# Optimization experiments

Measured on AMD Instinct MI355X. Metric: run time of the kernel, lower is better.

Reference implementation:

```python
import jax, jax.numpy as jnp
import numpy as np

B, C, H, W = 64, 128, 32, 32
GROUPS = 32
EPS = 1e-6
SCALE = 0.044194173824159216  # 1/sqrt(512), as hardcoded in the torch module


def setup_inputs() -> dict:
    key = jax.random.key(0)
    ks = jax.random.split(key, 12)
    s = 1.0 / np.sqrt(C)
    return {
        "x": jax.random.normal(ks[0], (B, C, H, W), dtype=jnp.float32),
        "gn_w": jax.random.normal(ks[1], (C,), dtype=jnp.float32) * 0.02 + 1.0,
        "gn_b": jax.random.normal(ks[2], (C,), dtype=jnp.float32) * 0.02,
        "wq": jax.random.uniform(ks[3], (C, C), jnp.float32, -s, s),
        "bq": jax.random.uniform(ks[4], (C,), jnp.float32, -s, s),
        "wk": jax.random.uniform(ks[5], (C, C), jnp.float32, -s, s),
        "bk": jax.random.uniform(ks[6], (C,), jnp.float32, -s, s),
        "wv": jax.random.uniform(ks[7], (C, C), jnp.float32, -s, s),
        "bv": jax.random.uniform(ks[8], (C,), jnp.float32, -s, s),
        "wo": jax.random.uniform(ks[9], (C, C), jnp.float32, -s, s),
        "bo": jax.random.uniform(ks[10], (C,), jnp.float32, -s, s),
    }


def reference(x, gn_w, gn_b, wq, bq, wk, bk, wv, bv, wo, bo):
    b = x.shape[0]
    res = x
    # GroupNorm(32 groups, 128 channels): normalize over (channels_per_group, H, W)
    xg = x.reshape(b, GROUPS, C // GROUPS, H * W)
    mean = xg.mean(axis=(2, 3), keepdims=True)
    var = xg.var(axis=(2, 3), keepdims=True)
    xn = (xg - mean) * jax.lax.rsqrt(var + EPS)
    xn = xn.reshape(b, C, H, W) * gn_w[:, None, None] + gn_b[:, None, None]
    # flatten spatial -> sequence: [b, S=1024, C=128]
    t = xn.reshape(b, C, H * W).transpose(0, 2, 1)
    q = t @ wq.T + bq
    k = t @ wk.T + bk
    v = t @ wv.T + bv
    att = jnp.einsum('bsc,btc->bst', q, k) * SCALE  # [b, S, S]
    att = jax.nn.softmax(att, axis=-1)
    o = jnp.einsum('bst,btc->bsc', att, v)
    o = o @ wo.T + bo
    out = o.transpose(0, 2, 1).reshape(b, C, H, W) + res
    return out
```

## Files before the change

### kernel.cpp

```cpp
#include <hip/hip_runtime.h>
#include <hip/hip_bf16.h>

#define BATCH 64
#define CCH 128
#define SEQ 1024
#define NG 32
#define EPSV 1e-6f
#define SCALEV 0.044194173824159216f
#define QPRE (0.044194173824159216f * 1.4426950408889634f)

typedef short v8s __attribute__((ext_vector_type(8)));
typedef short v4s __attribute__((ext_vector_type(4)));
typedef float v4f __attribute__((ext_vector_type(4)));
typedef int   v4i __attribute__((ext_vector_type(4)));
typedef unsigned short us;

__device__ __forceinline__ us f2bf(float f) {
    __hip_bfloat16 h = __float2bfloat16(f);
    return *reinterpret_cast<us*>(&h);
}

__device__ __forceinline__ int cvtpk(float lo, float hi) {
    int r;
    asm("v_cvt_pk_bf16_f32 %0, %1, %2" : "=v"(r) : "v"(lo), "v"(hi));
    return r;
}

#if __has_builtin(__builtin_amdgcn_exp2f)
#define EXP2F(x) __builtin_amdgcn_exp2f(x)
#else
#define EXP2F(x) exp2f(x)
#endif

#define MFMA16(a, b, c) __builtin_amdgcn_mfma_f32_16x16x32_bf16(a, b, c, 0, 0, 0)

__device__ __forceinline__ void gld_lds16(const us* g, us* l) {
    __builtin_amdgcn_global_load_lds(
        (const __attribute__((address_space(1))) void*)g,
        (__attribute__((address_space(3))) void*)l, 16, 0, 0);
}

__global__ void prep_gn(const float* __restrict__ wq, const float* __restrict__ wk,
                        const float* __restrict__ wv, const float* __restrict__ wo,
                        us* wbf, const float* __restrict__ x,
                        float* meanr, float* rstdr) {
    int tid = threadIdx.x;
    if (blockIdx.x < 256) {
        int i = blockIdx.x * 256 + tid;
        const float* srcs[4] = {wq, wk, wv, wo};
        wbf[i] = f2bf(srcs[i >> 14][i & 16383]);
        return;
    }
    int bg = blockIdx.x - 256;
    const float4* p = (const float4*)(x + (size_t)bg * (4 * SEQ));
    float s1 = 0.f, s2 = 0.f;
    #pragma unroll
    for (int i = 0; i < 4; i++) {
        float4 v = p[i * 256 + tid];
        s1 += v.x + v.y + v.z + v.w;
        s2 += v.x * v.x + v.y * v.y + v.z * v.z + v.w * v.w;
    }
    #pragma unroll
    for (int off = 32; off; off >>= 1) {
        s1 += __shfl_down(s1, off);
        s2 += __shfl_down(s2, off);
    }
    __shared__ float a1[4], a2[4];
    int w = tid >> 6, l = tid & 63;
    if (l == 0) { a1[w] = s1; a2[w] = s2; }
    __syncthreads();
    if (tid == 0) {
        float t1 = a1[0] + a1[1] + a1[2] + a1[3];
        float t2 = a2[0] + a2[1] + a2[2] + a2[3];
        float mean = t1 * (1.0f / (4 * SEQ));
        float var  = t2 * (1.0f / (4 * SEQ)) - mean * mean;
        meanr[bg] = mean;
        rstdr[bg] = rsqrtf(var + EPSV);
    }
}

__global__ __launch_bounds__(256, 4) void qkv_kernel(
    const float* __restrict__ x, const float* __restrict__ gn_w,
    const float* __restrict__ gn_b, const float* __restrict__ meanr,
    const float* __restrict__ rstdr, const us* __restrict__ wbf,
    const float* __restrict__ bq, const float* __restrict__ bk,
    const float* __restrict__ bv,
    us* Q, us* K, us* Vt)
{
    __shared__ us tls[9216];
    __shared__ float sa[CCH], sb[CCH];
    int b  = blockIdx.x >> 4;
    int s0 = (blockIdx.x & 15) * 64;
    int tid = threadIdx.x;
    const float* xb = x + (size_t)b * CCH * SEQ;

    if (tid < CCH) {
        int g = tid >> 2;
        float rs = rstdr[b * NG + g];
        float mu = meanr[b * NG + g];
        float a_ = rs * gn_w[tid];
        sa[tid] = a_;
        sb[tid] = gn_b[tid] - mu * a_;
    }
    __syncthreads();

    #pragma unroll
    for (int rep = 0; rep < 8; rep++) {
        int idx = rep * 256 + tid;
        int c = idx >> 4, s4 = idx & 15;
        float4 v = *(const float4*)&xb[c * SEQ + s0 + s4 * 4];
        float a_ = sa[c], b_ = sb[c];
        int sbase = s4 * 4;
        tls[(sbase + 0) * 136 + c] = f2bf(v.x * a_ + b_);
        tls[(sbase + 1) * 136 + c] = f2bf(v.y * a_ + b_);
        tls[(sbase + 2) * 136 + c] = f2bf(v.z * a_ + b_);
        tls[(sbase + 3) * 136 + c] = f2bf(v.w * a_ + b_);
    }
    __syncthreads();

    int w = tid >> 6, lane = tid & 63;
    int m = lane & 15, quad = lane >> 4;

    v8s a[4][4];
    #pragma unroll
    for (int st = 0; st < 4; st++)
        #pragma unroll
        for (int ch = 0; ch < 4; ch++)
            a[st][ch] = *(const v8s*)&tls[(st * 16 + m) * 136 + ch * 32 + quad * 8];
    __syncthreads();

    us* Qb = Q + (size_t)b * SEQ * CCH;
    us* Kb = K + (size_t)b * SEQ * CCH;
    us* Vb = Vt + (size_t)b * CCH * SEQ;

    #pragma unroll
    for (int o = 0; o < 3; o++) {
        const us* wmat = wbf + o * 16384;
        const float* bb = (o == 0) ? bq : (o == 1) ? bk : bv;
        #pragma unroll
        for (int t2 = 0; t2 < 2; t2++) {
            int T = (o * 2 + t2) * 4 + w;
            int ct = T & 7;
            int col = ct * 16 + m;
            v8s bfr[4];
            #pragma unroll
            for (int ch = 0; ch < 4; ch++)
                bfr[ch] = *(const v8s*)&wmat[(ct * 16 + m) * 128 + ch * 32 + quad * 8];
            float bias = bb[col];
            #pragma unroll
            for (int st = 0; st < 4; st++) {
                v4f acc = {0,0,0,0};
                #pragma unroll
                for (int ch = 0; ch < 4; ch++)
                    acc = MFMA16(a[st][ch], bfr[ch], acc);
                if (o < 2) {
                    #pragma unroll
                    for (int r = 0; r < 4; r++) {
                        float v = acc[r] + bias;
                        if (o == 0) v *= QPRE;
                        tls[(st * 16 + quad * 4 + r) * 136 + col] = f2bf(v);
                    }
                } else {
                    #pragma unroll
                    for (int r = 0; r < 4; r++)
                        tls[col * 72 + st * 16 + quad * 4 + r] = f2bf(acc[r] + bias);
                }
            }
        }
        __syncthreads();
        if (o < 2) {
            us* dst = (o == 0) ? Qb : Kb;
            #pragma unroll
            for (int rep = 0; rep < 4; rep++) {
                int idx = rep * 256 + tid;
                int row = idx >> 4, c8 = idx & 15;
                *(v8s*)&dst[(size_t)(s0 + row) * 128 + c8 * 8] =
                    *(const v8s*)&tls[row * 136 + c8 * 8];
            }
        } else {
            #pragma unroll
            for (int rep = 0; rep < 4; rep++) {
                int idx = rep * 256 + tid;
                int c = idx >> 3, c8 = idx & 7;
                *(v8s*)&Vb[(size_t)c * SEQ + s0 + c8 * 8] =
                    *(const v8s*)&tls[c * 72 + c8 * 8];
            }
        }
        if (o < 2) __syncthreads();
    }
}

__global__ __launch_bounds__(256, 3) void attn_kernel(
    const us* __restrict__ Q, const us* __restrict__ K,
    const us* __restrict__ Vt, const us* __restrict__ wbo,
    const float* __restrict__ bo, const float* __restrict__ x,
    float* __restrict__ out)
{
    __shared__ char smem_raw[49152];

    int i = blockIdx.x;
    int b  = (i & 7) * 8 + ((i >> 3) & 7);
    int qt = i >> 6;
    int tid = threadIdx.x;
    int w = tid >> 6, lane = tid & 63;
    int m = lane & 15, quad = lane >> 4;
    int qrow0 = qt * 128 + w * 32;
    const us* Qb = Q + (size_t)b * SEQ * CCH;
    const us* Kb = K + (size_t)b * SEQ * CCH;
    const us* Vb = Vt + (size_t)b * CCH * SEQ;

    v8s aq[2][4];
    #pragma unroll
    for (int st = 0; st < 2; st++)
        #pragma unroll
        for (int ch = 0; ch < 4; ch++)
            aq[st][ch] = *(const v8s*)&Qb[(size_t)(qrow0 + st * 16 + m) * 128 + ch * 32 + quad * 8];

    v4f oacc[2][8];
    #pragma unroll
    for (int st = 0; st < 2; st++)
        #pragma unroll
        for (int ct = 0; ct < 8; ct++) oacc[st][ct] = (v4f){0, 0, 0, 0};
    float lrun[2] = {0.f, 0.f};

    const us* kg[4]; const us* vg[4];
    int jb = w * 4;
    #pragma unroll
    for (int j4 = 0; j4 < 4; j4++) {
        int j = jb + j4;
        int kr = 4 * j + (lane >> 4);
        kg[j4] = Kb + (size_t)kr * 128 + ((lane & 15) ^ (kr & 15)) * 8;
        int vc = 8 * j + (lane >> 3);
        vg[j4] = Vb + (size_t)vc * SEQ + ((lane & 7) ^ (vc & 7)) * 8;
    }
    int idx0 = 2 * (quad & 1) * 16 + m;
    int idx1 = idx0 + 16;

    #pragma unroll
    for (int j4 = 0; j4 < 4; j4++) {
        gld_lds16(kg[j4], (us*)smem_raw + (jb + j4) * 512);
        gld_lds16(vg[j4], (us*)(smem_raw + 32768) + (jb + j4) * 512);
    }

    for (int kt = 0; kt < 16; kt++) {
        int kcur = (kt & 1) ? 16384 : 0;
        if (kt < 15) {
            #pragma unroll
            for (int j4 = 0; j4 < 4; j4++)
                gld_lds16(kg[j4] + (size_t)(kt + 1) * 8192,
                          (us*)(smem_raw + (kcur ^ 16384)) + (jb + j4) * 512);
            asm volatile("s_waitcnt vmcnt(4)" ::: "memory");
        } else {
            asm volatile("s_waitcnt vmcnt(0)" ::: "memory");
        }
        __builtin_amdgcn_s_barrier();

        const us* kl = (const us*)(smem_raw + kcur);
        const us* vl = (const us*)(smem_raw + 32768);

        __builtin_amdgcn_s_setprio(1);

        v4f acc0[4], acc1[4];
        int e[2][4][2];

        #define QK_STEP(c2) { \
            int krow = (c2) * 16 + m; \
            v4f A0 = {0,0,0,0}, A1 = {0,0,0,0}; \
            _Pragma("unroll") \
            for (int ch = 0; ch < 4; ch++) { \
                int chunk = (ch * 4 + quad) ^ (krow & 15); \
                v8s kb = *(const v8s*)&kl[krow * 128 + chunk * 8]; \
                A0 = MFMA16(kb, aq[0][ch], A0); \
                A1 = MFMA16(kb, aq[1][ch], A1); \
            } \
            acc0[c2] = A0; acc1[c2] = A1; }

        #define EXP_STEP(c2) { \
            float p0[4], p1[4]; \
            _Pragma("unroll") \
            for (int r = 0; r < 4; r++) { \
                p0[r] = EXP2F(acc0[c2][r]); \
                p1[r] = EXP2F(acc1[c2][r]); \
                lrun[0] += p0[r]; lrun[1] += p1[r]; \
            } \
            e[0][c2][0] = cvtpk(p0[0], p0[1]); e[0][c2][1] = cvtpk(p0[2], p0[3]); \
            e[1][c2][0] = cvtpk(p1[0], p1[1]); e[1][c2][1] = cvtpk(p1[2], p1[3]); }

        QK_STEP(0)
        QK_STEP(1)
        EXP_STEP(0)
        QK_STEP(2)
        EXP_STEP(1)
        QK_STEP(3)
        EXP_STEP(2)
        EXP_STEP(3)

        #define SHFL_STEP(kc2, paw) { \
            _Pragma("unroll") \
            for (int st = 0; st < 2; st++) { \
                int c0 = (quad < 2) ? e[st][2 * (kc2)][0] : e[st][2 * (kc2) + 1][0]; \
                int c1 = (quad < 2) ? e[st][2 * (kc2)][1] : e[st][2 * (kc2) + 1][1]; \
                v4i t; \
                t[0] = __shfl(c0, idx0); \
                t[1] = __shfl(c1, idx0); \
                t[2] = __shfl(c0, idx1); \
                t[3] = __shfl(c1, idx1); \
                paw[st] = __builtin_bit_cast(v8s, t); } }

        v8s pa0[2], pa1[2];
        SHFL_STEP(0, pa0)
        #pragma unroll
        for (int ct = 0; ct < 8; ct++) {
            int vrow = ct * 16 + m;
            int chunk = quad ^ (vrow & 7);
            v8s vb = *(const v8s*)&vl[vrow * 64 + chunk * 8];
            oacc[0][ct] = MFMA16(pa0[0], vb, oacc[0][ct]);
            oacc[1][ct] = MFMA16(pa0[1], vb, oacc[1][ct]);
        }
        SHFL_STEP(1, pa1)
        #pragma unroll
        for (int ct = 0; ct < 8; ct++) {
            int vrow = ct * 16 + m;
            int chunk = (4 + quad) ^ (vrow & 7);
            v8s vb = *(const v8s*)&vl[vrow * 64 + chunk * 8];
            oacc[0][ct] = MFMA16(pa1[0], vb, oacc[0][ct]);
            oacc[1][ct] = MFMA16(pa1[1], vb, oacc[1][ct]);
        }
        __builtin_amdgcn_s_setprio(0);
        #undef QK_STEP
        #undef EXP_STEP
        #undef SHFL_STEP

        __builtin_amdgcn_s_barrier();
        if (kt < 15) {
            #pragma unroll
            for (int j4 = 0; j4 < 4; j4++)
                gld_lds16(vg[j4] + (size_t)(kt + 1) * 64,
                          (us*)(smem_raw + 32768) + (jb + j4) * 512);
        }
    }

    float inv[2][4];
    #pragma unroll
    for (int st = 0; st < 2; st++) {
        float rs = lrun[st];
        rs += __shfl_xor(rs, 16);
        rs += __shfl_xor(rs, 32);
        #pragma unroll
        for (int r = 0; r < 4; r++)
            inv[st][r] = 1.0f / __shfl(rs, quad * 4 + r);
    }
    __syncthreads();
    us* olds = (us*)smem_raw;
    #pragma unroll
    for (int st = 0; st < 2; st++)
        #pragma unroll
        for (int ct = 0; ct < 8; ct++)
            #pragma unroll
            for (int r = 0; r < 4; r++)
                olds[(w * 32 + st * 16 + quad * 4 + r) * 136 + ct * 16 + m] =
                    f2bf(oacc[st][ct][r] * inv[st][r]);
    __syncthreads();

    const float* xb = x + (size_t)b * CCH * SEQ;
    float* ob = out + (size_t)b * CCH * SEQ;
    int sbase = qt * 128 + w * 32;
    v8s obf[2][4];
    #pragma unroll
    for (int st = 0; st < 2; st++)
        #pragma unroll
        for (int ch = 0; ch < 4; ch++)
            obf[st][ch] = *(const v8s*)&olds[(w * 32 + st * 16 + m) * 136 + ch * 32 + quad * 8];
    #pragma unroll
    for (int mt = 0; mt < 8; mt++) {
        v8s af[4];
        #pragma unroll
        for (int ch = 0; ch < 4; ch++)
            af[ch] = *(const v8s*)&wbo[(mt * 16 + m) * 128 + ch * 32 + quad * 8];
        #pragma unroll
        for (int st = 0; st < 2; st++) {
            v4f acc = {0,0,0,0};
            #pragma unroll
            for (int ch = 0; ch < 4; ch++)
                acc = MFMA16(af[ch], obf[st][ch], acc);
            #pragma unroll
            for (int r = 0; r < 4; r++) {
                int c = mt * 16 + quad * 4 + r;
                int idx = c * SEQ + sbase + st * 16 + m;
                ob[idx] = acc[r] + bo[c] + xb[idx];
            }
        }
    }
}

extern "C" void kernel_launch(void* const* d_in, const int* in_sizes, int n_in,
                              void* d_out, int out_size, void* d_ws, size_t ws_size,
                              hipStream_t stream) {
    const float* x    = (const float*)d_in[0];
    const float* gn_w = (const float*)d_in[1];
    const float* gn_b = (const float*)d_in[2];
    const float* wq   = (const float*)d_in[3];
    const float* bq   = (const float*)d_in[4];
    const float* wk   = (const float*)d_in[5];
    const float* bk   = (const float*)d_in[6];
    const float* wv   = (const float*)d_in[7];
    const float* bv   = (const float*)d_in[8];
    const float* wo   = (const float*)d_in[9];
    const float* bo   = (const float*)d_in[10];
    float* out = (float*)d_out;

    char* ws = (char*)d_ws;
    us* wbf      = (us*)ws;
    float* meanr = (float*)(ws + 131072);
    float* rstdr = (float*)(ws + 139264);
    us* Qbuf     = (us*)(ws + 147456);
    us* Kbuf     = (us*)(ws + 147456 + 16777216ull);
    us* Vtbuf    = (us*)(ws + 147456 + 2ull * 16777216ull);

    prep_gn<<<256 + BATCH * NG, 256, 0, stream>>>(wq, wk, wv, wo, wbf, x, meanr, rstdr);
    qkv_kernel<<<1024, 256, 0, stream>>>(x, gn_w, gn_b, meanr, rstdr, wbf,
                                         bq, bk, bv, Qbuf, Kbuf, Vtbuf);
    attn_kernel<<<512, 256, 0, stream>>>(Qbuf, Kbuf, Vtbuf, wbf + 3 * 16384,
                                         bo, x, out);
}
```

Baseline: 187.6 us.

## Split attention key range across two wave groups per block with cross-group merge

The attention kernel now launches 512 threads per block as two groups of four waves. Each group processes half of the key/value sequence with its own double-buffered K and V tiles in a 64KB LDS region. At the end, the row sums are combined through LDS and the partial output accumulators are summed, then normalized. This doubles the waves available to hide latency per query tile, at the cost of more LDS, extra barriers, a merge step, and a different occupancy limit.

```diff
diff --git a/kernel.cpp b/kernel.cpp
--- a/kernel.cpp
+++ b/kernel.cpp
@@ -190,21 +190,22 @@
     }
 }
 
-__global__ __launch_bounds__(256, 3) void attn_kernel(
+__global__ __launch_bounds__(512, 4) void attn_kernel(
     const us* __restrict__ Q, const us* __restrict__ K,
     const us* __restrict__ Vt, const us* __restrict__ wbo,
     const float* __restrict__ bo, const float* __restrict__ x,
     float* __restrict__ out)
 {
-    __shared__ char smem_raw[49152];
+    __shared__ char smem_raw[65536];
 
     int i = blockIdx.x;
     int b  = (i & 7) * 8 + ((i >> 3) & 7);
     int qt = i >> 6;
     int tid = threadIdx.x;
     int w = tid >> 6, lane = tid & 63;
+    int g = w >> 2, w4 = w & 3;
     int m = lane & 15, quad = lane >> 4;
-    int qrow0 = qt * 128 + w * 32;
+    int qrow0 = qt * 128 + w4 * 32;
     const us* Qb = Q + (size_t)b * SEQ * CCH;
     const us* Kb = K + (size_t)b * SEQ * CCH;
     const us* Vb = Vt + (size_t)b * CCH * SEQ;
@@ -223,45 +224,50 @@
         for (int ct = 0; ct < 8; ct++) oacc[st][ct] = (v4f){0, 0, 0, 0};
     float lrun[2] = {0.f, 0.f};
 
-    const us* kg[4]; const us* vg[4];
-    int jb = w * 4;
-    #pragma unroll
-    for (int j4 = 0; j4 < 4; j4++) {
-        int j = jb + j4;
+    const us* kg[2]; const us* vg[2];
+    int jb = w4 * 2;
+    #pragma unroll
+    for (int j2 = 0; j2 < 2; j2++) {
+        int j = jb + j2;
         int kr = 4 * j + (lane >> 4);
-        kg[j4] = Kb + (size_t)kr * 128 + ((lane & 15) ^ (kr & 15)) * 8;
-        int vc = 8 * j + (lane >> 3);
-        vg[j4] = Vb + (size_t)vc * SEQ + ((lane & 7) ^ (vc & 7)) * 8;
+        kg[j2] = Kb + (size_t)(g * 512 + kr) * 128 + ((lane & 15) ^ (kr & 15)) * 8;
+        int vc = 16 * j + (lane >> 2);
+        vg[j2] = Vb + (size_t)vc * SEQ + g * 512 + ((lane & 3) ^ (vc & 3)) * 8;
     }
     int idx0 = 2 * (quad & 1) * 16 + m;
     int idx1 = idx0 + 16;
-
-    #pragma unroll
-    for (int j4 = 0; j4 < 4; j4++) {
-        gld_lds16(kg[j4], (us*)smem_raw + (jb + j4) * 512);
-        gld_lds16(vg[j4], (us*)(smem_raw + 32768) + (jb + j4) * 512);
+    int gbase = g * 32768;
+
+    #pragma unroll
+    for (int j2 = 0; j2 < 2; j2++) {
+        gld_lds16(kg[j2], (us*)(smem_raw + gbase) + (jb + j2) * 512);
+        gld_lds16(vg[j2], (us*)(smem_raw + gbase + 16384) + (jb + j2) * 512);
     }
 
     for (int kt = 0; kt < 16; kt++) {
-        int kcur = (kt & 1) ? 16384 : 0;
+        int cb = (kt & 1) ? 8192 : 0;
         if (kt < 15) {
-            #pragma unroll
-            for (int j4 = 0; j4 < 4; j4++)
-                gld_lds16(kg[j4] + (size_t)(kt + 1) * 8192,
-                          (us*)(smem_raw + (kcur ^ 16384)) + (jb + j4) * 512);
+            int nb = cb ^ 8192;
+            #pragma unroll
+            for (int j2 = 0; j2 < 2; j2++) {
+                gld_lds16(kg[j2] + (size_t)(kt + 1) * 4096,
+                          (us*)(smem_raw + gbase + nb) + (jb + j2) * 512);
+                gld_lds16(vg[j2] + (size_t)(kt + 1) * 32,
+                          (us*)(smem_raw + gbase + 16384 + nb) + (jb + j2) * 512);
+            }
             asm volatile("s_waitcnt vmcnt(4)" ::: "memory");
         } else {
             asm volatile("s_waitcnt vmcnt(0)" ::: "memory");
         }
         __builtin_amdgcn_s_barrier();
 
-        const us* kl = (const us*)(smem_raw + kcur);
-        const us* vl = (const us*)(smem_raw + 32768);
+        const us* kl = (const us*)(smem_raw + gbase + cb);
+        const us* vl = (const us*)(smem_raw + gbase + 16384 + cb);
 
         __builtin_amdgcn_s_setprio(1);
 
-        v4f acc0[4], acc1[4];
-        int e[2][4][2];
+        v4f acc0[2], acc1[2];
+        int e[2][2][2];
 
         #define QK_STEP(c2) { \
             int krow = (c2) * 16 + m; \
@@ -269,9 +275,9 @@
             _Pragma("unroll") \
             for (int ch = 0; ch < 4; ch++) { \
                 int chunk = (ch * 4 + quad) ^ (krow & 15); \
-                v8s kb = *(const v8s*)&kl[krow * 128 + chunk * 8]; \
-                A0 = MFMA16(kb, aq[0][ch], A0); \
-                A1 = MFMA16(kb, aq[1][ch], A1); \
+                v8s kb2 = *(const v8s*)&kl[krow * 128 + chunk * 8]; \
+                A0 = MFMA16(kb2, aq[0][ch], A0); \
+                A1 = MFMA16(kb2, aq[1][ch], A1); \
             } \
             acc0[c2] = A0; acc1[c2] = A1; }
 
@@ -289,106 +295,117 @@
         QK_STEP(0)
         QK_STEP(1)
         EXP_STEP(0)
-        QK_STEP(2)
         EXP_STEP(1)
-        QK_STEP(3)
-        EXP_STEP(2)
-        EXP_STEP(3)
-
-        #define SHFL_STEP(kc2, paw) { \
-            _Pragma("unroll") \
-            for (int st = 0; st < 2; st++) { \
-                int c0 = (quad < 2) ? e[st][2 * (kc2)][0] : e[st][2 * (kc2) + 1][0]; \
-                int c1 = (quad < 2) ? e[st][2 * (kc2)][1] : e[st][2 * (kc2) + 1][1]; \
-                v4i t; \
-                t[0] = __shfl(c0, idx0); \
-                t[1] = __shfl(c1, idx0); \
-                t[2] = __shfl(c0, idx1); \
-                t[3] = __shfl(c1, idx1); \
-                paw[st] = __builtin_bit_cast(v8s, t); } }
-
-        v8s pa0[2], pa1[2];
-        SHFL_STEP(0, pa0)
+
+        v8s pa[2];
+        #pragma unroll
+        for (int st = 0; st < 2; st++) {
+            int c0 = (quad < 2) ? e[st][0][0] : e[st][1][0];
+            int c1 = (quad < 2) ? e[st][0][1] : e[st][1][1];
+            v4i t;
+            t[0] = __shfl(c0, idx0);
+            t[1] = __shfl(c1, idx0);
+            t[2] = __shfl(c0, idx1);
+            t[3] = __shfl(c1, idx1);
+            pa[st] = __builtin_bit_cast(v8s, t);
+        }
         #pragma unroll
         for (int ct = 0; ct < 8; ct++) {
             int vrow = ct * 16 + m;
-            int chunk = quad ^ (vrow & 7);
-            v8s vb = *(const v8s*)&vl[vrow * 64 + chunk * 8];
-            oacc[0][ct] = MFMA16(pa0[0], vb, oacc[0][ct]);
-            oacc[1][ct] = MFMA16(pa0[1], vb, oacc[1][ct]);
-        }
-        SHFL_STEP(1, pa1)
-        #pragma unroll
-        for (int ct = 0; ct < 8; ct++) {
-            int vrow = ct * 16 + m;
-            int chunk = (4 + quad) ^ (vrow & 7);
-            v8s vb = *(const v8s*)&vl[vrow * 64 + chunk * 8];
-            oacc[0][ct] = MFMA16(pa1[0], vb, oacc[0][ct]);
-            oacc[1][ct] = MFMA16(pa1[1], vb, oacc[1][ct]);
+            int chunk = quad ^ (vrow & 3);
+            v8s vb = *(const v8s*)&vl[vrow * 32 + chunk * 8];
+            oacc[0][ct] = MFMA16(pa[0], vb, oacc[0][ct]);
+            oacc[1][ct] = MFMA16(pa[1], vb, oacc[1][ct]);
         }
         __builtin_amdgcn_s_setprio(0);
         #undef QK_STEP
         #undef EXP_STEP
-        #undef SHFL_STEP
 
         __builtin_amdgcn_s_barrier();
-        if (kt < 15) {
-            #pragma unroll
-            for (int j4 = 0; j4 < 4; j4++)
-                gld_lds16(vg[j4] + (size_t)(kt + 1) * 64,
-                          (us*)(smem_raw + 32768) + (jb + j4) * 512);
-        }
-    }
-
-    float inv[2][4];
-    #pragma unroll
-    for (int st = 0; st < 2; st++) {
-        float rs = lrun[st];
-        rs += __shfl_xor(rs, 16);
-        rs += __shfl_xor(rs, 32);
-        #pragma unroll
-        for (int r = 0; r < 4; r++)
-            inv[st][r] = 1.0f / __shfl(rs, quad * 4 + r);
+    }
+
+    float rs0 = lrun[0]; rs0 += __shfl_xor(rs0, 16); rs0 += __shfl_xor(rs0, 32);
+    float rs1 = lrun[1]; rs1 += __shfl_xor(rs1, 16); rs1 += __shfl_xor(rs1, 32);
+    __syncthreads();
+    float* lf = (float*)smem_raw;
+    if (quad == 0) {
+        lf[g * 128 + w4 * 32 + m]      = rs0;
+        lf[g * 128 + w4 * 32 + 16 + m] = rs1;
+    }
+    __syncthreads();
+    v4f inv0, inv1;
+    {
+        v4f la = *(const v4f*)&lf[w4 * 32 + quad * 4];
+        v4f lb2 = *(const v4f*)&lf[128 + w4 * 32 + quad * 4];
+        #pragma unroll
+        for (int r = 0; r < 4; r++) inv0[r] = 1.0f / (la[r] + lb2[r]);
+        la = *(const v4f*)&lf[w4 * 32 + 16 + quad * 4];
+        lb2 = *(const v4f*)&lf[128 + w4 * 32 + 16 + quad * 4];
+        #pragma unroll
+        for (int r = 0; r < 4; r++) inv1[r] = 1.0f / (la[r] + lb2[r]);
+    }
+    __syncthreads();
+    float* Oa = (float*)smem_raw;
+    if (g == 0) {
+        #pragma unroll
+        for (int st = 0; st < 2; st++)
+            #pragma unroll
+            for (int ct = 0; ct < 8; ct++)
+                #pragma unroll
+                for (int r = 0; r < 4; r++)
+                    Oa[(w4 * 32 + st * 16 + quad * 4 + r) * 128 +
+                       (((ct * 16 + m)) ^ ((quad & 1) << 4))] = oacc[st][ct][r];
+    }
+    __syncthreads();
+    if (g == 1) {
+        #pragma unroll
+        for (int st = 0; st < 2; st++)
+            #pragma unroll
+            for (int ct = 0; ct < 8; ct++)
+                #pragma unroll
+                for (int r = 0; r < 4; r++) {
+                    float v = oacc[st][ct][r] +
+                        Oa[(w4 * 32 + st * 16 + quad * 4 + r) * 128 +
+                           (((ct * 16 + m)) ^ ((quad & 1) << 4))];
+                    oacc[st][ct][r] = v * (st == 0 ? inv0[r] : inv1[r]);
+                }
     }
     __syncthreads();
     us* olds = (us*)smem_raw;
-    #pragma unroll
-    for (int st = 0; st < 2; st++)
-        #pragma unroll
-        for (int ct = 0; ct < 8; ct++)
-            #pragma unroll
-            for (int r = 0; r < 4; r++)
-                olds[(w * 32 + st * 16 + quad * 4 + r) * 136 + ct * 16 + m] =
-                    f2bf(oacc[st][ct][r] * inv[st][r]);
+    if (g == 1) {
+        #pragma unroll
+        for (int st = 0; st < 2; st++)
+            #pragma unroll
+            for (int ct = 0; ct < 8; ct++)
+                #pragma unroll
+                for (int r = 0; r < 4; r++)
+                    olds[(w4 * 32 + st * 16 + quad * 4 + r) * 136 + ct * 16 + m] =
+                        f2bf(oacc[st][ct][r]);
+    }
     __syncthreads();
 
     const float* xb = x + (size_t)b * CCH * SEQ;
     float* ob = out + (size_t)b * CCH * SEQ;
-    int sbase = qt * 128 + w * 32;
-    v8s obf[2][4];
-    #pragma unroll
-    for (int st = 0; st < 2; st++)
-        #pragma unroll
-        for (int ch = 0; ch < 4; ch++)
-            obf[st][ch] = *(const v8s*)&olds[(w * 32 + st * 16 + m) * 136 + ch * 32 + quad * 8];
+    int sbase = qt * 128 + w * 16;
+    v8s obf[4];
+    #pragma unroll
+    for (int ch = 0; ch < 4; ch++)
+        obf[ch] = *(const v8s*)&olds[(w * 16 + m) * 136 + ch * 32 + quad * 8];
     #pragma unroll
     for (int mt = 0; mt < 8; mt++) {
         v8s af[4];
         #pragma unroll
         for (int ch = 0; ch < 4; ch++)
             af[ch] = *(const v8s*)&wbo[(mt * 16 + m) * 128 + ch * 32 + quad * 8];
-        #pragma unroll
-        for (int st = 0; st < 2; st++) {
-            v4f acc = {0,0,0,0};
-            #pragma unroll
-            for (int ch = 0; ch < 4; ch++)
-                acc = MFMA16(af[ch], obf[st][ch], acc);
-            #pragma unroll
-            for (int r = 0; r < 4; r++) {
-                int c = mt * 16 + quad * 4 + r;
-                int idx = c * SEQ + sbase + st * 16 + m;
-                ob[idx] = acc[r] + bo[c] + xb[idx];
-            }
+        v4f acc = {0,0,0,0};
+        #pragma unroll
+        for (int ch = 0; ch < 4; ch++)
+            acc = MFMA16(af[ch], obf[ch], acc);
+        #pragma unroll
+        for (int r = 0; r < 4; r++) {
+            int c = mt * 16 + quad * 4 + r;
+            int idx = c * SEQ + sbase + m;
+            ob[idx] = acc[r] + bo[c] + xb[idx];
         }
     }
 }
@@ -420,6 +437,6 @@
     prep_gn<<<256 + BATCH * NG, 256, 0, stream>>>(wq, wk, wv, wo, wbf, x, meanr, rstdr);
     qkv_kernel<<<1024, 256, 0, stream>>>(x, gn_w, gn_b, meanr, rstdr, wbf,
                                          bq, bk, bv, Qbuf, Kbuf, Vtbuf);
-    attn_kernel<<<512, 256, 0, stream>>>(Qbuf, Kbuf, Vtbuf, wbf + 3 * 16384,
+    attn_kernel<<<512, 512, 0, stream>>>(Qbuf, Kbuf, Vtbuf, wbf + 3 * 16384,
                                          bo, x, out);
 }
```

Measured after the change: 215.1 us. 1.15x slower.

## Load K fragments directly into registers and double-buffer V in LDS

Applied to the files above, without the earlier changes.

Each wave now reads its K tiles straight from global memory into a 4x4 register fragment array, prefetched partway through the previous iteration, so K no longer goes through LDS. The freed LDS holds a double buffer for V, and the V prefetch for the next tile is issued at the top of the loop instead of after the trailing barrier. This removes K LDS traffic and one synchronisation gap for V. In exchange, every wave loads the full K tile separately (four times the K reads from L2), register pressure rises, and the occupancy hint drops from 3 to 2 blocks per CU.

```diff
diff --git a/kernel.cpp b/kernel.cpp
--- a/kernel.cpp
+++ b/kernel.cpp
@@ -190,13 +190,13 @@
     }
 }
 
-__global__ __launch_bounds__(256, 3) void attn_kernel(
+__global__ __launch_bounds__(256, 2) void attn_kernel(
     const us* __restrict__ Q, const us* __restrict__ K,
     const us* __restrict__ Vt, const us* __restrict__ wbo,
     const float* __restrict__ bo, const float* __restrict__ x,
     float* __restrict__ out)
 {
-    __shared__ char smem_raw[49152];
+    __shared__ char smem_raw[34816];
 
     int i = blockIdx.x;
     int b  = (i & 7) * 8 + ((i >> 3) & 7);
@@ -223,40 +223,43 @@
         for (int ct = 0; ct < 8; ct++) oacc[st][ct] = (v4f){0, 0, 0, 0};
     float lrun[2] = {0.f, 0.f};
 
-    const us* kg[4]; const us* vg[4];
+    const us* vg[4];
     int jb = w * 4;
     #pragma unroll
     for (int j4 = 0; j4 < 4; j4++) {
         int j = jb + j4;
-        int kr = 4 * j + (lane >> 4);
-        kg[j4] = Kb + (size_t)kr * 128 + ((lane & 15) ^ (kr & 15)) * 8;
         int vc = 8 * j + (lane >> 3);
         vg[j4] = Vb + (size_t)vc * SEQ + ((lane & 7) ^ (vc & 7)) * 8;
     }
     int idx0 = 2 * (quad & 1) * 16 + m;
     int idx1 = idx0 + 16;
 
-    #pragma unroll
-    for (int j4 = 0; j4 < 4; j4++) {
-        gld_lds16(kg[j4], (us*)smem_raw + (jb + j4) * 512);
-        gld_lds16(vg[j4], (us*)(smem_raw + 32768) + (jb + j4) * 512);
-    }
+    const us* kbase = Kb + (size_t)m * 128 + quad * 8;
+
+    #pragma unroll
+    for (int j4 = 0; j4 < 4; j4++)
+        gld_lds16(vg[j4], (us*)smem_raw + (jb + j4) * 512);
+    v8s kf[4][4];
+    #pragma unroll
+    for (int c2 = 0; c2 < 4; c2++)
+        #pragma unroll
+        for (int ch = 0; ch < 4; ch++)
+            kf[c2][ch] = *(const v8s*)&kbase[c2 * 2048 + ch * 32];
 
     for (int kt = 0; kt < 16; kt++) {
-        int kcur = (kt & 1) ? 16384 : 0;
+        int cb = (kt & 1) ? 16384 : 0;
         if (kt < 15) {
             #pragma unroll
             for (int j4 = 0; j4 < 4; j4++)
-                gld_lds16(kg[j4] + (size_t)(kt + 1) * 8192,
-                          (us*)(smem_raw + (kcur ^ 16384)) + (jb + j4) * 512);
+                gld_lds16(vg[j4] + (size_t)(kt + 1) * 64,
+                          (us*)(smem_raw + (cb ^ 16384)) + (jb + j4) * 512);
             asm volatile("s_waitcnt vmcnt(4)" ::: "memory");
         } else {
             asm volatile("s_waitcnt vmcnt(0)" ::: "memory");
         }
         __builtin_amdgcn_s_barrier();
 
-        const us* kl = (const us*)(smem_raw + kcur);
-        const us* vl = (const us*)(smem_raw + 32768);
+        const us* vl = (const us*)(smem_raw + cb);
 
         __builtin_amdgcn_s_setprio(1);
 
@@ -264,14 +267,11 @@
         int e[2][4][2];
 
         #define QK_STEP(c2) { \
-            int krow = (c2) * 16 + m; \
             v4f A0 = {0,0,0,0}, A1 = {0,0,0,0}; \
             _Pragma("unroll") \
             for (int ch = 0; ch < 4; ch++) { \
-                int chunk = (ch * 4 + quad) ^ (krow & 15); \
-                v8s kb = *(const v8s*)&kl[krow * 128 + chunk * 8]; \
-                A0 = MFMA16(kb, aq[0][ch], A0); \
-                A1 = MFMA16(kb, aq[1][ch], A1); \
+                A0 = MFMA16(kf[c2][ch], aq[0][ch], A0); \
+                A1 = MFMA16(kf[c2][ch], aq[1][ch], A1); \
             } \
             acc0[c2] = A0; acc1[c2] = A1; }
 
@@ -292,6 +292,16 @@
         QK_STEP(2)
         EXP_STEP(1)
         QK_STEP(3)
+
+        if (kt < 15) {
+            const us* kpn = kbase + (size_t)(kt + 1) * 8192;
+            #pragma unroll
+            for (int c2 = 0; c2 < 4; c2++)
+                #pragma unroll
+                for (int ch = 0; ch < 4; ch++)
+                    kf[c2][ch] = *(const v8s*)&kpn[c2 * 2048 + ch * 32];
+        }
+
         EXP_STEP(2)
         EXP_STEP(3)
 
@@ -332,12 +342,6 @@
         #undef SHFL_STEP
 
         __builtin_amdgcn_s_barrier();
-        if (kt < 15) {
-            #pragma unroll
-            for (int j4 = 0; j4 < 4; j4++)
-                gld_lds16(vg[j4] + (size_t)(kt + 1) * 64,
-                          (us*)(smem_raw + 32768) + (jb + j4) * 512);
-        }
     }
 
     float inv[2][4];
```

Result: slower. 208.5 us (+11.1%).
